# Optimization experiments

Measured on AMD Instinct MI355X. Metric: run time of the kernel, lower is better.

Reference implementation:

```python
import jax, jax.numpy as jnp
import numpy as np

NF = 64      # feature channels of h
K = 3        # dynamic filter spatial size (padding=1 in source implies k=3)
FACTOR = 4   # pixel-unshuffle factor


def shuffle_down(x, f):
    # torch pixel_unshuffle: (B,C,H*f,W*f) -> (B,C*f*f,H,W)
    B, C, H, W = x.shape
    x = x.reshape(B, C, H // f, f, W // f, f)
    x = x.transpose(0, 1, 3, 5, 2, 4)
    return x.reshape(B, C * f * f, H // f, W // f)


def _patches3x3(x):
    # x: (B,C,H,W) -> (B,C,9,H,W): zero-padded 3x3 neighborhoods, row-major taps,
    # identical to the identity-filter grouped conv (im2col) in the source.
    H, W = x.shape[-2], x.shape[-1]
    xp = jnp.pad(x, ((0, 0), (0, 0), (1, 1), (1, 1)))
    shifts = [xp[:, :, dy:dy + H, dx:dx + W] for dy in range(K) for dx in range(K)]
    return jnp.stack(shifts, axis=2)


def setup_inputs() -> dict:
    key = jax.random.key(0)
    k1, k2, k3, k4 = jax.random.split(key, 4)
    B, H, W = 2, 256, 256
    h = jax.random.normal(k1, (B, NF, H, W), dtype=jnp.float32)
    i_t = jax.random.normal(k2, (B, 3, H * FACTOR, W * FACTOR), dtype=jnp.float32)
    conv_w = jax.random.normal(k3, (K * K, 3 * FACTOR ** 2, K, K), dtype=jnp.float32) * 0.05
    conv_b = jax.random.normal(k4, (K * K,), dtype=jnp.float32) * 0.05
    return {"h": h, "i_t": i_t, "conv_w": conv_w, "conv_b": conv_b}


def reference(h, i_t, conv_w, conv_b):
    # predict per-pixel 3x3 filters from the shuffled-down guidance frame
    x = shuffle_down(i_t, FACTOR)  # (B, 48, H, W)
    f = jax.lax.conv_general_dilated(
        x, conv_w, window_strides=(1, 1), padding=((1, 1), (1, 1)),
        dimension_numbers=("NCHW", "OIHW", "NCHW"))
    filters = jax.nn.relu(f + conv_b[None, :, None, None])  # (B, 9, H, W)

    # dynamic per-pixel conv: same 3x3 filter applied to every channel of h
    patches = _patches3x3(h)  # (B, nf, 9, H, W)
    out = jnp.einsum("bcfhw,bfhw->bchw", patches, filters)  # (B, nf, H, W)
    return out
```

## Files before the change

### kernel.cpp

```cpp
#include <hip/hip_runtime.h>

#define HSZ 256
#define WSZ 256
#define NFC 64
#define PLANE (HSZ * WSZ)

typedef __attribute__((ext_vector_type(8))) short short8;
typedef __attribute__((ext_vector_type(4))) float f32x4;

__device__ inline unsigned short f2bf(float f) {
    unsigned u = __builtin_bit_cast(unsigned, f);
    return (unsigned short)((u + 0x7fffu + ((u >> 16) & 1u)) >> 16);
}

__global__ __launch_bounds__(256, 4) void fused_dynfilter_v3(
    const float* __restrict__ hbuf,
    const float* __restrict__ i_t,
    const float* __restrict__ wbuf,
    const float* __restrict__ bias,
    float* __restrict__ out)
{
    __shared__ __align__(16) unsigned char smem[28096];
    unsigned short* const xs  = (unsigned short*)smem;
    unsigned short* const lwT = (unsigned short*)(smem + 20160);
    float* const lf = (float*)(smem + 20160);
    float* const hs = (float*)smem;

    const int tid = threadIdx.x;

    const int lin = blockIdx.x + 16 * (blockIdx.y + 32 * blockIdx.z);
    const int q   = ((int)gridDim.z * 512) >> 3;
    const int nid = (lin & 7) * q + (lin >> 3);
    const int b   = nid >> 9;
    const int rem = nid & 511;
    const int X0  = (rem & 15) * 16;
    const int Y0  = (rem >> 4) * 8;

    const int lane = tid & 63;
    const int l15  = lane & 15;
    const int kg   = lane >> 4;
    const int wv   = tid >> 6;

    const float bv = (l15 < 9) ? bias[l15] : 0.f;
    const float* itb = i_t + (size_t)b * 3 * (PLANE * 16);

    {
        float4 lreg[9]; int sdst[9];
#pragma unroll
        for (int k = 0; k < 9; ++k) {
            const int v = tid + 256 * k;
            const int sp = v / 12, t = v - sp * 12;
            const int c3 = t >> 2, fy = t & 3;
            const int ly = sp / 18, lx = sp - ly * 18;
            const int Y = Y0 - 1 + ly, X = X0 - 1 + lx;
            float4 val = make_float4(0.f, 0.f, 0.f, 0.f);
            if (v < 2160 && (unsigned)Y < HSZ && (unsigned)X < WSZ)
                val = *(const float4*)(itb + ((size_t)c3 * 1024 + (4 * Y + fy)) * 1024 + 4 * X);
            lreg[k] = val;
            sdst[k] = (v < 2160) ? (sp * 56 + t * 4) : -1;
        }
#pragma unroll
        for (int k = 0; k < 9; ++k)
            if (sdst[k] >= 0) {
                ushort4 u{f2bf(lreg[k].x), f2bf(lreg[k].y), f2bf(lreg[k].z), f2bf(lreg[k].w)};
                *(ushort4*)(xs + sdst[k]) = u;
            }
    }

    {
        float4 wr[4];
#pragma unroll
        for (int k = 0; k < 4; ++k) {
            const int v = tid + 256 * k;
            wr[k] = (v < 972) ? *(const float4*)(wbuf + (size_t)v * 4)
                              : make_float4(0.f, 0.f, 0.f, 0.f);
        }
#pragma unroll
        for (int k = 0; k < 4; ++k) {
            const int v = tid + 256 * k;
            if (v < 972) {
                const float e[4] = {wr[k].x, wr[k].y, wr[k].z, wr[k].w};
#pragma unroll
                for (int j = 0; j < 4; ++j) {
                    const int n  = v * 4 + j;
                    const int oc = n / 432;
                    const int r  = n - 432 * oc;
                    const int ic = r / 9;
                    const int kk = r - 9 * ic;
                    lwT[oc * 440 + kk * 48 + ic] = f2bf(e[j]);
                }
            }
        }
    }

    __syncthreads();

    short8 wf[14];
    {
        const unsigned short* lwb = lwT + l15 * 440 + kg * 8;
#pragma unroll
        for (int kb = 0; kb < 14; ++kb) {
            short8 w = {0, 0, 0, 0, 0, 0, 0, 0};
            if (l15 < 9 && !(kb == 13 && kg >= 2))
                w = *(const short8*)(lwb + kb * 32);
            wf[kb] = w;
        }
    }

    f32x4 acc0 = {0.f, 0.f, 0.f, 0.f}, acc1 = acc0;
#pragma unroll
    for (int kb = 0; kb < 14; ++kb) {
        const int k0 = kb * 32 + kg * 8;
        int off = 0;
        if (k0 < 432) {
            const int kk = k0 / 48, ic0 = k0 - 48 * kk;
            const int ky = kk / 3, kx = kk - 3 * ky;
            off = ((2 * wv + ky) * 18 + l15 + kx) * 56 + ic0;
        }
        short8 a0 = *(const short8*)(xs + off);
        short8 a1 = *(const short8*)(xs + off + 1008);
        acc0 = __builtin_amdgcn_mfma_f32_16x16x32_bf16(a0, wf[kb], acc0, 0, 0, 0);
        acc1 = __builtin_amdgcn_mfma_f32_16x16x32_bf16(a1, wf[kb], acc1, 0, 0, 0);
    }

    __syncthreads();

    if (l15 < 9) {
#pragma unroll
        for (int t = 0; t < 2; ++t) {
            const int py = 2 * wv + t;
            const f32x4 A = t ? acc1 : acc0;
#pragma unroll
            for (int r = 0; r < 4; ++r)
                lf[l15 * 128 + py * 16 + (kg * 4 + r)] = fmaxf(A[r] + bv, 0.f);
        }
    }

    const int pq  = tid & 3;
    const int pyA = (tid >> 2) & 7;
    const int clo = tid >> 5;

    float4 h0reg[2]; int h0dst[2];
    {
        const float* hp = hbuf + (size_t)b * NFC * PLANE;
#pragma unroll
        for (int k = 0; k < 2; ++k) {
            const int v = tid + 256 * k;
            float4 val = make_float4(0.f, 0.f, 0.f, 0.f);
            int d = -1;
            if (v < 480) {
                const int c = v / 60, r = v - 60 * c;
                const int row = r / 6, xq = r - 6 * row;
                const int Y = Y0 - 1 + row, X4 = X0 - 4 + xq * 4;
                if ((unsigned)Y < HSZ && (unsigned)X4 < WSZ)
                    val = *(const float4*)(hp + (size_t)c * PLANE + (size_t)Y * WSZ + X4);
                d = c * 240 + row * 24 + xq * 4;
            }
            h0reg[k] = val; h0dst[k] = d;
        }
    }

    __syncthreads();

    float4 flt[9];
#pragma unroll
    for (int oc = 0; oc < 9; ++oc)
        flt[oc] = *(const float4*)(lf + oc * 128 + pyA * 16 + pq * 4);

#pragma unroll
    for (int k = 0; k < 2; ++k)
        if (h0dst[k] >= 0) *(float4*)(hs + h0dst[k]) = h0reg[k];

    __syncthreads();

#pragma unroll
    for (int cg = 0; cg < 8; ++cg) {
        const int buf = cg & 1;

        float4 nreg[2]; int ndst[2];
        if (cg < 7) {
            const float* hp = hbuf + ((size_t)b * NFC + (cg + 1) * 8) * PLANE;
#pragma unroll
            for (int k = 0; k < 2; ++k) {
                const int v = tid + 256 * k;
                float4 val = make_float4(0.f, 0.f, 0.f, 0.f);
                int d = -1;
                if (v < 480) {
                    const int c = v / 60, r = v - 60 * c;
                    const int row = r / 6, xq = r - 6 * row;
                    const int Y = Y0 - 1 + row, X4 = X0 - 4 + xq * 4;
                    if ((unsigned)Y < HSZ && (unsigned)X4 < WSZ)
                        val = *(const float4*)(hp + (size_t)c * PLANE + (size_t)Y * WSZ + X4);
                    d = c * 240 + row * 24 + xq * 4;
                }
                nreg[k] = val; ndst[k] = d;
            }
        }

        float a[4];
#pragma unroll
        for (int j = 0; j < 4; ++j) a[j] = 0.f;

        const float* pl = hs + buf * 1920 + clo * 240;
#pragma unroll
        for (int ky = 0; ky < 3; ++ky) {
            const float* rp = pl + (pyA + ky) * 24 + pq * 4;
            const float4 w0 = *(const float4*)rp;
            const float4 w1 = *(const float4*)(rp + 4);
            const float  w8 = rp[8];
            const float vs[9] = {w0.x, w0.y, w0.z, w0.w, w1.x, w1.y, w1.z, w1.w, w8};
#pragma unroll
            for (int kx = 0; kx < 3; ++kx)
#pragma unroll
                for (int j = 0; j < 4; ++j)
                    a[j] = fmaf(vs[3 + kx + j], flt[ky * 3 + kx][j], a[j]);
        }

        const int ch = cg * 8 + clo;
        *(float4*)(out + ((size_t)b * NFC + ch) * PLANE
                       + (size_t)(Y0 + pyA) * WSZ + X0 + pq * 4)
            = make_float4(a[0], a[1], a[2], a[3]);

        if (cg < 7) {
            float* hb = hs + (buf ^ 1) * 1920;
#pragma unroll
            for (int k = 0; k < 2; ++k)
                if (ndst[k] >= 0) *(float4*)(hb + ndst[k]) = nreg[k];
            __syncthreads();
        }
    }
}

extern "C" void kernel_launch(void* const* d_in, const int* in_sizes, int n_in,
                              void* d_out, int out_size, void* d_ws, size_t ws_size,
                              hipStream_t stream) {
    const float* h      = (const float*)d_in[0];
    const float* i_t    = (const float*)d_in[1];
    const float* conv_w = (const float*)d_in[2];
    const float* conv_b = (const float*)d_in[3];
    float* out = (float*)d_out;

    const int B = in_sizes[0] / (NFC * PLANE);
    dim3 grid(WSZ / 16, HSZ / 8, B);
    fused_dynfilter_v3<<<grid, 256, 0, stream>>>(h, i_t, conv_w, conv_b, out);
}
```

Before: 116.9 us.

## Read h neighborhoods directly from global memory instead of LDS double buffering

```diff
diff --git a/kernel.cpp b/kernel.cpp
--- a/kernel.cpp
+++ b/kernel.cpp
@@ -13,18 +13,17 @@
     return (unsigned short)((u + 0x7fffu + ((u >> 16) & 1u)) >> 16);
 }
 
-__global__ __launch_bounds__(256, 4) void fused_dynfilter_v3(
+__global__ __launch_bounds__(256, 4) void fused_dynfilter_v4(
     const float* __restrict__ hbuf,
     const float* __restrict__ i_t,
     const float* __restrict__ wbuf,
     const float* __restrict__ bias,
     float* __restrict__ out)
 {
-    __shared__ __align__(16) unsigned char smem[28096];
+    __shared__ __align__(16) unsigned char smem[32688];
     unsigned short* const xs  = (unsigned short*)smem;
     unsigned short* const lwT = (unsigned short*)(smem + 20160);
-    float* const lf = (float*)(smem + 20160);
-    float* const hs = (float*)smem;
+    float* const lf = (float*)(smem + 28080);
 
     const int tid = threadIdx.x;
 
@@ -123,8 +122,6 @@
         acc1 = __builtin_amdgcn_mfma_f32_16x16x32_bf16(a1, wf[kb], acc1, 0, 0, 0);
     }
 
-    __syncthreads();
-
     if (l15 < 9) {
 #pragma unroll
         for (int t = 0; t < 2; ++t) {
@@ -136,98 +133,54 @@
         }
     }
 
+    __syncthreads();
+
     const int pq  = tid & 3;
     const int pyA = (tid >> 2) & 7;
     const int clo = tid >> 5;
-
-    float4 h0reg[2]; int h0dst[2];
-    {
-        const float* hp = hbuf + (size_t)b * NFC * PLANE;
-#pragma unroll
-        for (int k = 0; k < 2; ++k) {
-            const int v = tid + 256 * k;
-            float4 val = make_float4(0.f, 0.f, 0.f, 0.f);
-            int d = -1;
-            if (v < 480) {
-                const int c = v / 60, r = v - 60 * c;
-                const int row = r / 6, xq = r - 6 * row;
-                const int Y = Y0 - 1 + row, X4 = X0 - 4 + xq * 4;
-                if ((unsigned)Y < HSZ && (unsigned)X4 < WSZ)
-                    val = *(const float4*)(hp + (size_t)c * PLANE + (size_t)Y * WSZ + X4);
-                d = c * 240 + row * 24 + xq * 4;
-            }
-            h0reg[k] = val; h0dst[k] = d;
-        }
-    }
-
-    __syncthreads();
 
     float4 flt[9];
 #pragma unroll
     for (int oc = 0; oc < 9; ++oc)
         flt[oc] = *(const float4*)(lf + oc * 128 + pyA * 16 + pq * 4);
 
+    const int col0 = X0 + pq * 4;
+    const int Yc   = Y0 + pyA;
+    const bool gl  = (col0 > 0);
+    const bool gr  = (col0 < WSZ - 4);
+
+    bool rg[3]; int roff[3];
 #pragma unroll
-    for (int k = 0; k < 2; ++k)
-        if (h0dst[k] >= 0) *(float4*)(hs + h0dst[k]) = h0reg[k];
+    for (int ky = 0; ky < 3; ++ky) {
+        const int Y = Yc - 1 + ky;
+        rg[ky]   = ((unsigned)Y < HSZ);
+        roff[ky] = Y * WSZ + col0;
+    }
 
-    __syncthreads();
+    const float* hp0 = hbuf + ((size_t)b * NFC + clo) * PLANE;
+    float* outp = out + ((size_t)b * NFC + clo) * PLANE + (size_t)Yc * WSZ + col0;
 
-#pragma unroll
+#pragma unroll 2
     for (int cg = 0; cg < 8; ++cg) {
-        const int buf = cg & 1;
+        const float* p = hp0 + (size_t)cg * 8 * PLANE;
 
-        float4 nreg[2]; int ndst[2];
-        if (cg < 7) {
-            const float* hp = hbuf + ((size_t)b * NFC + (cg + 1) * 8) * PLANE;
-#pragma unroll
-            for (int k = 0; k < 2; ++k) {
-                const int v = tid + 256 * k;
-                float4 val = make_float4(0.f, 0.f, 0.f, 0.f);
-                int d = -1;
-                if (v < 480) {
-                    const int c = v / 60, r = v - 60 * c;
-                    const int row = r / 6, xq = r - 6 * row;
-                    const int Y = Y0 - 1 + row, X4 = X0 - 4 + xq * 4;
-                    if ((unsigned)Y < HSZ && (unsigned)X4 < WSZ)
-                        val = *(const float4*)(hp + (size_t)c * PLANE + (size_t)Y * WSZ + X4);
-                    d = c * 240 + row * 24 + xq * 4;
-                }
-                nreg[k] = val; ndst[k] = d;
-            }
-        }
-
-        float a[4];
-#pragma unroll
-        for (int j = 0; j < 4; ++j) a[j] = 0.f;
-
-        const float* pl = hs + buf * 1920 + clo * 240;
+        float a[4] = {0.f, 0.f, 0.f, 0.f};
 #pragma unroll
         for (int ky = 0; ky < 3; ++ky) {
-            const float* rp = pl + (pyA + ky) * 24 + pq * 4;
-            const float4 w0 = *(const float4*)rp;
-            const float4 w1 = *(const float4*)(rp + 4);
-            const float  w8 = rp[8];
-            const float vs[9] = {w0.x, w0.y, w0.z, w0.w, w1.x, w1.y, w1.z, w1.w, w8};
+            float  sl = (rg[ky] && gl) ? p[roff[ky] - 1] : 0.f;
+            float4 fm = rg[ky] ? *(const float4*)(p + roff[ky])
+                               : make_float4(0.f, 0.f, 0.f, 0.f);
+            float  sr = (rg[ky] && gr) ? p[roff[ky] + 4] : 0.f;
+            const float v6[6] = {sl, fm.x, fm.y, fm.z, fm.w, sr};
 #pragma unroll
             for (int kx = 0; kx < 3; ++kx)
 #pragma unroll
                 for (int j = 0; j < 4; ++j)
-                    a[j] = fmaf(vs[3 + kx + j], flt[ky * 3 + kx][j], a[j]);
+                    a[j] = fmaf(v6[kx + j], flt[ky * 3 + kx][j], a[j]);
         }
 
-        const int ch = cg * 8 + clo;
-        *(float4*)(out + ((size_t)b * NFC + ch) * PLANE
-                       + (size_t)(Y0 + pyA) * WSZ + X0 + pq * 4)
+        *(float4*)(outp + (size_t)cg * 8 * PLANE)
             = make_float4(a[0], a[1], a[2], a[3]);
-
-        if (cg < 7) {
-            float* hb = hs + (buf ^ 1) * 1920;
-#pragma unroll
-            for (int k = 0; k < 2; ++k)
-                if (ndst[k] >= 0) *(float4*)(hb + ndst[k]) = nreg[k];
-            __syncthreads();
-        }
     }
 }
 
@@ -242,5 +195,5 @@
 
     const int B = in_sizes[0] / (NFC * PLANE);
     dim3 grid(WSZ / 16, HSZ / 8, B);
-    fused_dynfilter_v3<<<grid, 256, 0, stream>>>(h, i_t, conv_w, conv_b, out);
+    fused_dynfilter_v4<<<grid, 256, 0, stream>>>(h, i_t, conv_w, conv_b, out);
 }
```

New measurement: 130.1 us. 11.3% more time.
